# Performance work log

Hardware: AMD Instinct MI355X
Metric: run time of the kernel (lower is better)

## Reference

```python
import jax, jax.numpy as jnp
import numpy as np

HIDDEN = 2048
Q_HEADS = 16
KV_HEADS = 4
HEAD_DIM = HIDDEN // Q_HEADS  # 128
GROUPS = Q_HEADS // KV_HEADS  # 4


def setup_inputs() -> dict:
    key = jax.random.key(0)
    ks = jax.random.split(key, 5)
    scale = 1.0 / np.sqrt(HIDDEN)
    x = jax.random.normal(ks[0], (1, 4096, HIDDEN), dtype=jnp.float32)
    # nn.Linear weights stored as [out_features, in_features]
    Wq = jax.random.uniform(ks[1], (Q_HEADS * HEAD_DIM, HIDDEN), jnp.float32, -scale, scale)
    Wk = jax.random.uniform(ks[2], (KV_HEADS * HEAD_DIM, HIDDEN), jnp.float32, -scale, scale)
    Wv = jax.random.uniform(ks[3], (KV_HEADS * HEAD_DIM, HIDDEN), jnp.float32, -scale, scale)
    Wo = jax.random.uniform(ks[4], (HIDDEN, HIDDEN), jnp.float32, -scale, scale)
    return {"x": x, "Wq": Wq, "Wk": Wk, "Wv": Wv, "Wo": Wo}


def reference(x, Wq, Wk, Wv, Wo):
    b, s, _ = x.shape
    norm = jnp.asarray(np.sqrt(HEAD_DIM), x.dtype)
    # Projections (Linear without bias: x @ W.T)
    q = (x @ Wq.T).reshape(b, s, KV_HEADS, GROUPS, HEAD_DIM)  # group q heads by shared kv head
    k = (x @ Wk.T).reshape(b, s, KV_HEADS, HEAD_DIM)
    v = (x @ Wv.T).reshape(b, s, KV_HEADS, HEAD_DIM)
    # Scores: repeat_interleave of KV is equivalent to sharing k across the g axis
    att = jnp.einsum('bskgd,btkd->bkgst', q, k) / norm  # [b,kv,groups,s,s]
    att = jax.nn.softmax(att, axis=-1)
    out = jnp.einsum('bkgst,btkd->bskgd', att, v).reshape(b, s, HIDDEN)
    return out @ Wo.T
```

## Files before the change

### kernel.cpp

```cpp
#include <hip/hip_runtime.h>
#include <stdint.h>

#define SEQ 4096
#define HID 2048

typedef __attribute__((ext_vector_type(8))) short short8;
typedef __attribute__((ext_vector_type(4))) float f32x4;
typedef __attribute__((ext_vector_type(16))) float f32x16;
typedef unsigned int u32;
typedef __attribute__((ext_vector_type(4))) u32 u32x4;

__device__ __forceinline__ short bf16_rne(float f) {
  u32 u = __builtin_bit_cast(u32, f);
  u += 0x7FFFu + ((u >> 16) & 1u);
  return (short)(u >> 16);
}

__device__ __forceinline__ void gload16(const void* gp, void* lp) {
  __builtin_amdgcn_global_load_lds(
      (const __attribute__((address_space(1))) u32*)(uintptr_t)gp,
      (__attribute__((address_space(3))) u32*)(uintptr_t)lp, 16, 0, 0);
}

__global__ __launch_bounds__(256) void cast_bf16(const float* __restrict__ in,
                                                 short* __restrict__ out, int n8) {
  int i = blockIdx.x * 256 + threadIdx.x;
  if (i >= n8) return;
  const f32x4* p = (const f32x4*)in + (size_t)i * 2;
  f32x4 a = p[0], b = p[1];
  short8 o;
#pragma unroll
  for (int j = 0; j < 4; ++j) { o[j] = bf16_rne(a[j]); o[j + 4] = bf16_rne(b[j]); }
  *((short8*)out + i) = o;
}

__global__ __launch_bounds__(256) void transpose_v(const short* __restrict__ qkv,
                                                   short* __restrict__ vt) {
  __shared__ __align__(16) short tile[64][72];
  int rb = blockIdx.x * 64, cb = blockIdx.y * 64;
  int tid = threadIdx.x;
  int tr = tid >> 3, tc = (tid & 7) * 8;
#pragma unroll
  for (int i = 0; i < 2; ++i)
    *(short8*)&tile[tr + i * 32][tc] =
        *(const short8*)&qkv[(size_t)(rb + tr + i * 32) * 3072 + 2560 + cb + tc];
  __syncthreads();
#pragma unroll
  for (int i = 0; i < 2; ++i) {
    int c = tr + i * 32;
    short8 v;
#pragma unroll
    for (int j = 0; j < 8; ++j) {
      int pos = tc + j;
      int tl = (pos & ~15) | (pos & 3) | ((pos & 4) << 1) | ((pos & 8) >> 1);
      v[j] = tile[tl][c];
    }
    *(short8*)&vt[(size_t)(cb + c) * SEQ + rb + tc] = v;
  }
}

template <typename CT>
__global__ __launch_bounds__(256, 2) void gemm_nt(const short* __restrict__ A,
                                                  const short* __restrict__ B,
                                                  CT* __restrict__ C, int M, int N, int K) {
  __shared__ __align__(16) short As[128 * 32];
  __shared__ __align__(16) short Bs[128 * 32];
  int tid = threadIdx.x, wave = tid >> 6, lane = tid & 63;
  int lr = lane & 15, lg = lane >> 4;
  int wr = wave >> 1, wc = wave & 1;
  size_t rowA0 = (size_t)blockIdx.y * 128, colB0 = (size_t)blockIdx.x * 128;
  f32x4 acc[4][4] = {};

  for (int kt = 0; kt < K; kt += 32) {
#pragma unroll
    for (int c = 0; c < 2; ++c) {
      int chunk = wave * 2 + c;
      int row = chunk * 16 + (lane >> 2);
      int col = (lane & 3) * 8;
      gload16(A + (rowA0 + row) * (size_t)K + kt + col, &As[chunk * 512]);
      gload16(B + (colB0 + row) * (size_t)K + kt + col, &Bs[chunk * 512]);
    }
    __syncthreads();
    short8 a[4], b[4];
#pragma unroll
    for (int i = 0; i < 4; ++i) {
      a[i] = *(const short8*)&As[(wr * 64 + i * 16 + lr) * 32 + lg * 8];
      b[i] = *(const short8*)&Bs[(wc * 64 + i * 16 + lr) * 32 + lg * 8];
    }
#pragma unroll
    for (int i = 0; i < 4; ++i)
#pragma unroll
      for (int j = 0; j < 4; ++j)
        acc[i][j] = __builtin_amdgcn_mfma_f32_16x16x32_bf16(a[i], b[j], acc[i][j], 0, 0, 0);
    __syncthreads();
  }
#pragma unroll
  for (int i = 0; i < 4; ++i)
#pragma unroll
    for (int j = 0; j < 4; ++j)
#pragma unroll
      for (int r = 0; r < 4; ++r) {
        size_t row = rowA0 + wr * 64 + i * 16 + lg * 4 + r;
        size_t col = colB0 + wc * 64 + j * 16 + lr;
        if constexpr (sizeof(CT) == 2) C[row * N + col] = (CT)bf16_rne(acc[i][j][r]);
        else C[row * N + col] = acc[i][j][r];
      }
}

__global__ __launch_bounds__(256, 2) void attn_kernel(const short* __restrict__ QKV,
                                                      const short* __restrict__ Vt,
                                                      short* __restrict__ Oat) {
  __shared__ __align__(16) short Ks[2][4096];
  __shared__ __align__(16) short Vs[2][4096];
  int tid = threadIdx.x, wave = tid >> 6, lane = tid & 63;
  int l31 = lane & 31, hi = lane >> 5;
  int h = blockIdx.y, kv = h >> 2;
  int q0 = blockIdx.x * 128 + wave * 32;

  short8 qf[8];
#pragma unroll
  for (int kb = 0; kb < 8; ++kb)
    qf[kb] = *(const short8*)&QKV[(size_t)(q0 + l31) * 3072 + h * 128 + kb * 16 + hi * 8];

  f32x16 oacc[4] = {};
  float m_run = -1e30f, lsum = 0.f;

  const float sc = 1.44269504089f * 0.08838834764831845f;
  const float THR_S = 60.f;
  const short* Kbase = QKV + 2048 + kv * 128;

  auto stageK = [&](int b, int t0) {
#pragma unroll
    for (int cc = 0; cc < 2; ++cc) {
      int c = wave * 2 + cc;
      gload16(Kbase + (size_t)(t0 + l31) * 3072 + c * 16 + hi * 8, &Ks[b][c * 512]);
    }
  };
  auto stageV = [&](int b, int t0) {
#pragma unroll
    for (int cc = 0; cc < 2; ++cc) {
      int c = wave * 2 + cc;
      int d = (c & 1) * 64 + lane;
      gload16(Vt + (size_t)(kv * 128 + d) * SEQ + t0 + (c >> 1) * 8, &Vs[b][c * 512]);
    }
  };

  stageK(0, 0);
  stageV(0, 0);
  __syncthreads();
  int buf = 0;

  for (int t0 = 0; t0 < SEQ; t0 += 32) {
    int tn = (t0 + 32 < SEQ) ? t0 + 32 : 0;
    stageK(buf ^ 1, tn);
    stageV(buf ^ 1, tn);

    f32x16 sacc = {};
    __builtin_amdgcn_s_setprio(1);
#pragma unroll
    for (int kb = 0; kb < 8; ++kb) {
      short8 kf = *(const short8*)&Ks[buf][((kb * 2 + hi) * 32 + l31) * 8];
      sacc = __builtin_amdgcn_mfma_f32_32x32x16_bf16(kf, qf[kb], sacc, 0, 0, 0);
    }
    __builtin_amdgcn_s_setprio(0);

    float vmax = fmaxf(sacc[0], sacc[1]);
#pragma unroll
    for (int r = 2; r < 16; ++r) vmax = fmaxf(vmax, sacc[r]);
    if (__any(vmax > m_run + THR_S)) {
      float mnew = fmaxf(fmaxf(vmax, __shfl_xor(vmax, 32)), m_run);
      float corr = __builtin_amdgcn_exp2f((m_run - mnew) * sc);
      lsum *= corr;
      m_run = mnew;
#pragma unroll
      for (int nb = 0; nb < 4; ++nb) oacc[nb] *= corr;
    }

    float msc = m_run * sc;
    float ps = 0.f;
    u32 w[8];
#pragma unroll
    for (int i = 0; i < 8; ++i) {
      float p0 = __builtin_amdgcn_exp2f(sacc[2 * i] * sc - msc);
      float p1 = __builtin_amdgcn_exp2f(sacc[2 * i + 1] * sc - msc);
      ps += p0 + p1;
      asm("v_cvt_pk_bf16_f32 %0, %1, %2" : "=v"(w[i]) : "v"(p0), "v"(p1));
    }
    lsum += ps;
    short8 pa0 = __builtin_bit_cast(short8, (u32x4){w[0], w[1], w[2], w[3]});
    short8 pa1 = __builtin_bit_cast(short8, (u32x4){w[4], w[5], w[6], w[7]});

    __builtin_amdgcn_s_setprio(1);
#pragma unroll
    for (int nb = 0; nb < 4; ++nb) {
      short8 v0 = *(const short8*)&Vs[buf][((hi)*128 + nb * 32 + l31) * 8];
      oacc[nb] = __builtin_amdgcn_mfma_f32_32x32x16_bf16(pa0, v0, oacc[nb], 0, 0, 0);
      short8 v1 = *(const short8*)&Vs[buf][((2 + hi) * 128 + nb * 32 + l31) * 8];
      oacc[nb] = __builtin_amdgcn_mfma_f32_32x32x16_bf16(pa1, v1, oacc[nb], 0, 0, 0);
    }
    __builtin_amdgcn_s_setprio(0);

    __syncthreads();
    buf ^= 1;
  }

  lsum += __shfl_xor(lsum, 32);
  float linv = 1.f / lsum;
#pragma unroll
  for (int r = 0; r < 16; ++r) {
    int qrow = (r & 3) + 8 * (r >> 2) + 4 * hi;
    float lr_ = __shfl(linv, qrow);
#pragma unroll
    for (int nb = 0; nb < 4; ++nb)
      Oat[(size_t)(q0 + qrow) * HID + h * 128 + nb * 32 + l31] = bf16_rne(oacc[nb][r] * lr_);
  }
}

extern "C" void kernel_launch(void* const* d_in, const int* in_sizes, int n_in,
                              void* d_out, int out_size, void* d_ws, size_t ws_size,
                              hipStream_t stream) {
  const float* x = (const float*)d_in[0];
  const float* Wq = (const float*)d_in[1];
  const float* Wk = (const float*)d_in[2];
  const float* Wv = (const float*)d_in[3];
  const float* Wo = (const float*)d_in[4];
  float* out = (float*)d_out;
  char* ws = (char*)d_ws;

  short* xb = (short*)(ws);
  short* wqkv = (short*)(ws + (16u << 20));
  short* wob = (short*)(ws + (28u << 20));
  short* qkv = (short*)(ws + (36u << 20));
  short* vt = wqkv;
  short* oat = xb;

  cast_bf16<<<4096, 256, 0, stream>>>(x, xb, 1048576);
  cast_bf16<<<2048, 256, 0, stream>>>(Wq, wqkv, 524288);
  cast_bf16<<<512, 256, 0, stream>>>(Wk, wqkv + (size_t)2048 * 2048, 131072);
  cast_bf16<<<512, 256, 0, stream>>>(Wv, wqkv + (size_t)2560 * 2048, 131072);
  cast_bf16<<<2048, 256, 0, stream>>>(Wo, wob, 524288);

  gemm_nt<short><<<dim3(24, 32), 256, 0, stream>>>(xb, wqkv, qkv, 4096, 3072, 2048);
  transpose_v<<<dim3(64, 8), 256, 0, stream>>>(qkv, vt);
  attn_kernel<<<dim3(32, 16), 256, 0, stream>>>(qkv, vt, oat);
  gemm_nt<float><<<dim3(16, 32), 256, 0, stream>>>(oat, wob, out, 4096, HID, 2048);
}
```

Baseline: 286.6 us.

## Software-pipeline attention with triple-buffered K/V and QK^T one tile ahead

```diff
diff --git a/kernel.cpp b/kernel.cpp
--- a/kernel.cpp
+++ b/kernel.cpp
@@ -110,8 +110,8 @@
 __global__ __launch_bounds__(256, 2) void attn_kernel(const short* __restrict__ QKV,
                                                       const short* __restrict__ Vt,
                                                       short* __restrict__ Oat) {
-  __shared__ __align__(16) short Ks[2][4096];
-  __shared__ __align__(16) short Vs[2][4096];
+  __shared__ __align__(16) short Ks[3 * 4096];
+  __shared__ __align__(16) short Vs[3 * 4096];
   int tid = threadIdx.x, wave = tid >> 6, lane = tid & 63;
   int l31 = lane & 31, hi = lane >> 5;
   int h = blockIdx.y, kv = h >> 2;
@@ -128,45 +128,44 @@
   const float sc = 1.44269504089f * 0.08838834764831845f;
   const float THR_S = 60.f;
   const short* Kbase = QKV + 2048 + kv * 128;
-
-  auto stageK = [&](int b, int t0) {
+  const short* Vbase = Vt + (size_t)(kv * 128) * SEQ;
+
+  auto stageK = [&](int bo, int tile) {
+    int t0 = tile * 32;
 #pragma unroll
     for (int cc = 0; cc < 2; ++cc) {
       int c = wave * 2 + cc;
-      gload16(Kbase + (size_t)(t0 + l31) * 3072 + c * 16 + hi * 8, &Ks[b][c * 512]);
-    }
-  };
-  auto stageV = [&](int b, int t0) {
+      gload16(Kbase + (size_t)(t0 + l31) * 3072 + c * 16 + hi * 8, &Ks[bo + c * 512]);
+    }
+  };
+  auto stageV = [&](int bo, int tile) {
+    int t0 = tile * 32;
 #pragma unroll
     for (int cc = 0; cc < 2; ++cc) {
       int c = wave * 2 + cc;
       int d = (c & 1) * 64 + lane;
-      gload16(Vt + (size_t)(kv * 128 + d) * SEQ + t0 + (c >> 1) * 8, &Vs[b][c * 512]);
-    }
-  };
-
-  stageK(0, 0);
-  stageV(0, 0);
-  __syncthreads();
-  int buf = 0;
-
-  for (int t0 = 0; t0 < SEQ; t0 += 32) {
-    int tn = (t0 + 32 < SEQ) ? t0 + 32 : 0;
-    stageK(buf ^ 1, tn);
-    stageV(buf ^ 1, tn);
-
-    f32x16 sacc = {};
+      gload16(Vbase + (size_t)d * SEQ + t0 + (c >> 1) * 8, &Vs[bo + c * 512]);
+    }
+  };
+
+  auto qkt = [&](int bo, f32x16& s) {
+    s = (f32x16){};
     __builtin_amdgcn_s_setprio(1);
 #pragma unroll
     for (int kb = 0; kb < 8; ++kb) {
-      short8 kf = *(const short8*)&Ks[buf][((kb * 2 + hi) * 32 + l31) * 8];
-      sacc = __builtin_amdgcn_mfma_f32_32x32x16_bf16(kf, qf[kb], sacc, 0, 0, 0);
+      short8 kf = *(const short8*)&Ks[bo + ((kb * 2 + hi) * 32 + l31) * 8];
+      s = __builtin_amdgcn_mfma_f32_32x32x16_bf16(kf, qf[kb], s, 0, 0, 0);
     }
     __builtin_amdgcn_s_setprio(0);
-
-    float vmax = fmaxf(sacc[0], sacc[1]);
-#pragma unroll
-    for (int r = 2; r < 16; ++r) vmax = fmaxf(vmax, sacc[r]);
+  };
+
+  auto smpv = [&](int bo, f32x16& s) {
+    float t0m = fmaxf(fmaxf(s[0], s[1]), s[2]);
+    float t1m = fmaxf(fmaxf(s[3], s[4]), s[5]);
+    float t2m = fmaxf(fmaxf(s[6], s[7]), s[8]);
+    float t3m = fmaxf(fmaxf(s[9], s[10]), s[11]);
+    float t4m = fmaxf(fmaxf(s[12], s[13]), s[14]);
+    float vmax = fmaxf(fmaxf(fmaxf(t0m, t1m), t2m), fmaxf(fmaxf(t3m, t4m), s[15]));
     if (__any(vmax > m_run + THR_S)) {
       float mnew = fmaxf(fmaxf(vmax, __shfl_xor(vmax, 32)), m_run);
       float corr = __builtin_amdgcn_exp2f((m_run - mnew) * sc);
@@ -175,34 +174,55 @@
 #pragma unroll
       for (int nb = 0; nb < 4; ++nb) oacc[nb] *= corr;
     }
-
     float msc = m_run * sc;
-    float ps = 0.f;
+    float pp[8];
     u32 w[8];
 #pragma unroll
     for (int i = 0; i < 8; ++i) {
-      float p0 = __builtin_amdgcn_exp2f(sacc[2 * i] * sc - msc);
-      float p1 = __builtin_amdgcn_exp2f(sacc[2 * i + 1] * sc - msc);
-      ps += p0 + p1;
+      float p0 = __builtin_amdgcn_exp2f(s[2 * i] * sc - msc);
+      float p1 = __builtin_amdgcn_exp2f(s[2 * i + 1] * sc - msc);
+      pp[i] = p0 + p1;
       asm("v_cvt_pk_bf16_f32 %0, %1, %2" : "=v"(w[i]) : "v"(p0), "v"(p1));
     }
-    lsum += ps;
+    lsum += ((pp[0] + pp[1]) + (pp[2] + pp[3])) + ((pp[4] + pp[5]) + (pp[6] + pp[7]));
     short8 pa0 = __builtin_bit_cast(short8, (u32x4){w[0], w[1], w[2], w[3]});
     short8 pa1 = __builtin_bit_cast(short8, (u32x4){w[4], w[5], w[6], w[7]});
-
     __builtin_amdgcn_s_setprio(1);
 #pragma unroll
     for (int nb = 0; nb < 4; ++nb) {
-      short8 v0 = *(const short8*)&Vs[buf][((hi)*128 + nb * 32 + l31) * 8];
+      short8 v0 = *(const short8*)&Vs[bo + ((hi)*128 + nb * 32 + l31) * 8];
       oacc[nb] = __builtin_amdgcn_mfma_f32_32x32x16_bf16(pa0, v0, oacc[nb], 0, 0, 0);
-      short8 v1 = *(const short8*)&Vs[buf][((2 + hi) * 128 + nb * 32 + l31) * 8];
+      short8 v1 = *(const short8*)&Vs[bo + ((2 + hi) * 128 + nb * 32 + l31) * 8];
       oacc[nb] = __builtin_amdgcn_mfma_f32_32x32x16_bf16(pa1, v1, oacc[nb], 0, 0, 0);
     }
     __builtin_amdgcn_s_setprio(0);
-
-    __syncthreads();
-    buf ^= 1;
-  }
+  };
+
+  const int NT = SEQ / 32;
+  int r0 = 0, r1 = 4096, r2 = 8192;
+
+  stageK(r0, 0); stageV(r0, 0);
+  stageK(r1, 1); stageV(r1, 1);
+  __syncthreads();
+  f32x16 sA, sB;
+  qkt(r0, sB);
+
+#define PERIOD(I, SNEW, SCUR)                               \
+  {                                                         \
+    int ti2 = ((I) + 2 > NT - 1) ? NT - 1 : (I) + 2;        \
+    stageK(r2, ti2);                                        \
+    stageV(r2, ti2);                                        \
+    qkt(r1, SNEW);  \
+    smpv(r0, SCUR);             \
+    __syncthreads();                                        \
+    int tmp_ = r0; r0 = r1; r1 = r2; r2 = tmp_;             \
+  }
+
+  for (int i = 0; i < NT; i += 2) {
+    PERIOD(i, sA, sB);
+    PERIOD(i + 1, sB, sA);
+  }
+#undef PERIOD
 
   lsum += __shfl_xor(lsum, 32);
   float linv = 1.f / lsum;
```

New measurement: 288.7 us. About the same (+0.7%).
